# Optimization experiments

Hardware: AMD Instinct MI355X
Metric: run time of the kernel (lower is better)

## Reference

```python
import jax, jax.numpy as jnp
import numpy as np

N, D, F = 20000, 16, 3  # nodes, receptive-field size (degree), feature dim


def setup_inputs() -> dict:
    key = jax.random.key(0)
    k1, k2 = jax.random.split(key)
    # per-node feature tensors: first CCN layer, parts[i]={i}, so tensors[i] is [1,1,F] -> squeezed to [F]
    tensors = jax.random.normal(k1, (N, F), dtype=jnp.float32)
    # padded receptive fields: neigh[i] = child node indices with adjM[i, j] == 1
    neigh = jnp.sort(jax.random.randint(k2, (N, D), 0, N), axis=1)
    return {"tensors": tensors, "neigh": neigh}


def reference(tensors, neigh):
    # new_parts[i] = ordered union of children's (singleton) parts = sorted neighbor ids
    new_parts = jnp.sort(neigh, axis=1)  # [N, D]
    # chi[i, c, a] = 1 iff new_parts[i][a] == parts[neigh[i,c]][0] == neigh[i,c]
    # (the alternativePermutationMatrix_AToB in1d test, for singleton child parts)
    chi = (new_parts[:, None, :] == neigh[:, :, None]).astype(tensors.dtype)  # [N, D(child c), D(slot a)]
    # gather each child's feature tensor T[j,k,s] with j=k=1 -> [N, D, F]
    feat = tensors[neigh]
    # promotion einsum 'aj,bk,jks->abs' with |j|=|k|=1, batched over node i and child c
    promotions = jnp.einsum('nca,ncb,ncs->ncabs', chi, chi, feat)  # [N, D, D, D, F]
    return promotions, new_parts
```

## Files before the change

kernel.cpp:

```cpp
#include <hip/hip_runtime.h>


constexpr int NN = 20000;
constexpr int DD = 16;
constexpr int FF = 3;
constexpr int PROMO_PER_NODE = DD * DD * DD * FF;
constexpr long long PROMO_TOTAL = (long long)NN * PROMO_PER_NODE;

__global__ __launch_bounds__(192) void ccn_promote_kernel(
    const float* __restrict__ tensors,
    const int* __restrict__ neigh,
    float* __restrict__ out)
{
    const int n = blockIdx.x;
    const int t = threadIdx.x;

    __shared__ int   nv[DD];
    __shared__ float fv[DD][4];

    if (t < DD) {
        const int id = neigh[n * DD + t];
        nv[t] = id;
        out[(size_t)PROMO_TOTAL + (size_t)n * DD + t] = (float)id;
        const float* src = tensors + (size_t)id * FF;
        fv[t][0] = src[0];
        fv[t][1] = src[1];
        fv[t][2] = src[2];
        fv[t][3] = 0.0f;
    }
    __syncthreads();

    const int a  = t / 12;
    const int k  = t % 12;
    const int e0 = 4 * k;

    const int s0 = (e0 + 0) % 3, b0 = (e0 + 0) / 3;
    const int s1 = (e0 + 1) % 3, b1 = (e0 + 1) / 3;
    const int s2 = (e0 + 2) % 3, b2 = (e0 + 2) / 3;
    const int s3 = (e0 + 3) % 3, b3 = (e0 + 3) / 3;

    const int nva  = nv[a];
    const int nvb0 = nv[b0];
    const int nvb1 = nv[b1];
    const int nvb2 = nv[b2];
    const int nvb3 = nv[b3];

    int nvc_r[DD];
#pragma unroll
    for (int i = 0; i < DD; ++i) nvc_r[i] = nv[i];

    float4* outv = reinterpret_cast<float4*>(out + (size_t)n * PROMO_PER_NODE) + t;

#pragma unroll
    for (int c = 0; c < DD; ++c) {
        const int  nvc = nvc_r[c];
        const bool ca  = (nva == nvc);
        float4 v;
        v.x = (ca && (nvb0 == nvc)) ? fv[c][s0] : 0.0f;
        v.y = (ca && (nvb1 == nvc)) ? fv[c][s1] : 0.0f;
        v.z = (ca && (nvb2 == nvc)) ? fv[c][s2] : 0.0f;
        v.w = (ca && (nvb3 == nvc)) ? fv[c][s3] : 0.0f;
        outv[c * 192] = v;
    }
}

extern "C" void kernel_launch(void* const* d_in, const int* in_sizes, int n_in,
                              void* d_out, int out_size, void* d_ws, size_t ws_size,
                              hipStream_t stream) {
    const float* tensors = (const float*)d_in[0];
    const int*   neigh   = (const int*)d_in[1];
    float*       out     = (float*)d_out;

    ccn_promote_kernel<<<NN, 192, 0, stream>>>(tensors, neigh, out);
}
```

Before: 962.3 us.

## Split promotion into bulk nontemporal zero-fill and sparse nonzero scatter

Replaces the single dense-output kernel with two kernels. The first is a grid-stride kernel that zero-fills the promotion tensor using nontemporal vector stores. The second writes only the sparse nonzero entries where slot a, b and child c share the same neighbor id. This strips the per-element compare/select work out of the bulk write path and aims to stream zeros at full bandwidth. The cost is an extra kernel launch, a separate grid of small scattered scalar writes, and the output having to be serialized between the two kernels.

Result: slower. 1.036 ms (+7.7%).

```diff
diff --git a/kernel.cpp b/kernel.cpp
--- a/kernel.cpp
+++ b/kernel.cpp
@@ -6,8 +6,24 @@
 constexpr int FF = 3;
 constexpr int PROMO_PER_NODE = DD * DD * DD * FF;
 constexpr long long PROMO_TOTAL = (long long)NN * PROMO_PER_NODE;
+constexpr long long PROMO_V4 = PROMO_TOTAL / 4;
 
-__global__ __launch_bounds__(192) void ccn_promote_kernel(
+typedef float v4f __attribute__((ext_vector_type(4)));
+
+constexpr int ZBLOCKS  = 2048;
+constexpr int ZTHREADS = 256;
+
+__global__ __launch_bounds__(ZTHREADS) void zero_promotions(float* __restrict__ out)
+{
+    const v4f z = {0.0f, 0.0f, 0.0f, 0.0f};
+    v4f* o = reinterpret_cast<v4f*>(out);
+    const long long stride = (long long)ZBLOCKS * ZTHREADS;
+    for (long long i = (long long)blockIdx.x * ZTHREADS + threadIdx.x;
+         i < PROMO_V4; i += stride)
+        __builtin_nontemporal_store(z, o + i);
+}
+
+__global__ __launch_bounds__(256) void scatter_nonzeros(
     const float* __restrict__ tensors,
     const int* __restrict__ neigh,
     float* __restrict__ out)
@@ -15,52 +31,31 @@
     const int n = blockIdx.x;
     const int t = threadIdx.x;
 
-    __shared__ int   nv[DD];
-    __shared__ float fv[DD][4];
-
+    __shared__ int nv[DD];
     if (t < DD) {
         const int id = neigh[n * DD + t];
         nv[t] = id;
         out[(size_t)PROMO_TOTAL + (size_t)n * DD + t] = (float)id;
-        const float* src = tensors + (size_t)id * FF;
-        fv[t][0] = src[0];
-        fv[t][1] = src[1];
-        fv[t][2] = src[2];
-        fv[t][3] = 0.0f;
     }
     __syncthreads();
 
-    const int a  = t / 12;
-    const int k  = t % 12;
-    const int e0 = 4 * k;
+    const int c   = t >> 4;
+    const int a   = t & 15;
+    const int nvc = nv[c];
 
-    const int s0 = (e0 + 0) % 3, b0 = (e0 + 0) / 3;
-    const int s1 = (e0 + 1) % 3, b1 = (e0 + 1) / 3;
-    const int s2 = (e0 + 2) % 3, b2 = (e0 + 2) / 3;
-    const int s3 = (e0 + 3) % 3, b3 = (e0 + 3) / 3;
-
-    const int nva  = nv[a];
-    const int nvb0 = nv[b0];
-    const int nvb1 = nv[b1];
-    const int nvb2 = nv[b2];
-    const int nvb3 = nv[b3];
-
-    int nvc_r[DD];
+    if (nv[a] == nvc) {
+        const float f0 = tensors[(size_t)nvc * FF + 0];
+        const float f1 = tensors[(size_t)nvc * FF + 1];
+        const float f2 = tensors[(size_t)nvc * FF + 2];
+        float* base = out + (size_t)n * PROMO_PER_NODE + (size_t)((c * DD + a) * DD) * FF;
 #pragma unroll
-    for (int i = 0; i < DD; ++i) nvc_r[i] = nv[i];
-
-    float4* outv = reinterpret_cast<float4*>(out + (size_t)n * PROMO_PER_NODE) + t;
-
-#pragma unroll
-    for (int c = 0; c < DD; ++c) {
-        const int  nvc = nvc_r[c];
-        const bool ca  = (nva == nvc);
-        float4 v;
-        v.x = (ca && (nvb0 == nvc)) ? fv[c][s0] : 0.0f;
-        v.y = (ca && (nvb1 == nvc)) ? fv[c][s1] : 0.0f;
-        v.z = (ca && (nvb2 == nvc)) ? fv[c][s2] : 0.0f;
-        v.w = (ca && (nvb3 == nvc)) ? fv[c][s3] : 0.0f;
-        outv[c * 192] = v;
+        for (int b = 0; b < DD; ++b) {
+            if (nv[b] == nvc) {
+                base[b * FF + 0] = f0;
+                base[b * FF + 1] = f1;
+                base[b * FF + 2] = f2;
+            }
+        }
     }
 }
 
@@ -71,5 +66,6 @@
     const int*   neigh   = (const int*)d_in[1];
     float*       out     = (float*)d_out;
 
-    ccn_promote_kernel<<<NN, 192, 0, stream>>>(tensors, neigh, out);
+    zero_promotions<<<ZBLOCKS, ZTHREADS, 0, stream>>>(out);
+    scatter_nonzeros<<<NN, 256, 0, stream>>>(tensors, neigh, out);
 }
```
